# Kernel tuning notes

Hardware: AMD Instinct MI355X
Metric: run time of the kernel (lower is better)

The kernel has to match this reference:

```python
import jax, jax.numpy as jnp
import numpy as np

N_NODES = 50000
N_EDGES = 800000
HIDDEN = 100
NUM_TASKS = 128
NUM_GRAPHS = 2000
ATOM_DIMS = [119, 5, 12, 12, 10, 6, 6, 2, 2]  # OGB full_atom_feature_dims
EPS = 1e-16  # stands in for PyG's clamp(min=0) so that pow(-1) stays finite


def setup_inputs() -> dict:
    key = jax.random.key(0)
    ks = jax.random.split(key, 8)
    x = jax.random.randint(ks[0], (N_NODES, 9), 0, 2, dtype=jnp.int32)
    edge_index = jax.random.randint(ks[1], (2, N_EDGES), 0, N_NODES, dtype=jnp.int32)
    batch = jnp.sort(jax.random.randint(ks[2], (N_NODES,), 0, NUM_GRAPHS, dtype=jnp.int32))
    s = 1.0 / np.sqrt(HIDDEN)
    atom_emb = jax.random.normal(ks[3], (sum(ATOM_DIMS), HIDDEN), jnp.float32)
    W1 = jax.random.normal(ks[4], (HIDDEN, HIDDEN), jnp.float32) * s
    b1 = jnp.zeros((HIDDEN,), jnp.float32)
    W2 = jax.random.normal(ks[5], (HIDDEN, HIDDEN), jnp.float32) * s
    b2 = jnp.zeros((HIDDEN,), jnp.float32)
    Wlin = jax.random.normal(ks[6], (HIDDEN, NUM_TASKS), jnp.float32) * s
    blin = jnp.zeros((NUM_TASKS,), jnp.float32)
    return dict(x=x, edge_index=edge_index, batch=batch, atom_emb=atom_emb,
                W1=W1, b1=b1, W2=W2, b2=b2, Wlin=Wlin, blin=blin)


def reference(x, edge_index, batch, atom_emb, W1, b1, W2, b2, Wlin, blin):
    # --- AtomEncoder: sum of per-feature categorical embeddings ---
    offsets = jnp.asarray(np.concatenate([[0], np.cumsum(ATOM_DIMS)[:-1]]), jnp.int32)
    h = jnp.take(atom_emb, x + offsets[None, :], axis=0).sum(axis=1)  # [N, H]

    # --- GCN normalization with self-loops (gcn_norm, edge_weight=None) ---
    loops = jnp.arange(N_NODES, dtype=edge_index.dtype)
    row = jnp.concatenate([edge_index[0], loops])  # source
    col = jnp.concatenate([edge_index[1], loops])  # target
    ew = jnp.ones(row.shape[0], jnp.float32)
    deg = jax.ops.segment_sum(ew, col, num_segments=N_NODES)  # in-degree incl self-loop
    dinv = jnp.where(deg > 0, deg ** -0.5, 0.0)
    norm = dinv[row] * ew * dinv[col]  # [E+N]
    cnt = jnp.maximum(deg, 1.0)  # messages per target node (for mean)

    def gcn_conv(h, W, b):
        msg = norm[:, None] * (h @ W)[row]  # [E+N, H]
        # PowerMeanAggregation(p=-1): clamp(0,100).pow(-1) -> mean -> clamp(0,100).pow(-1)
        msg = jnp.clip(msg, EPS, 100.0) ** (-1.0)
        agg = jax.ops.segment_sum(msg, col, num_segments=N_NODES) / cnt[:, None]
        return jnp.clip(agg, EPS, 100.0) ** (-1.0) + b

    h = jax.nn.relu(gcn_conv(h, W1, b1))
    h = gcn_conv(h, W2, b2)

    # --- global_mean_pool over batch ---
    gcnt = jax.ops.segment_sum(jnp.ones((N_NODES,), jnp.float32), batch, num_segments=NUM_GRAPHS)
    pooled = jax.ops.segment_sum(h, batch, num_segments=NUM_GRAPHS) / jnp.maximum(gcnt, 1.0)[:, None]

    return pooled @ Wlin + blin  # [NUM_GRAPHS, NUM_TASKS]
```

## Files before the change

kernel.cpp:

```cpp
#include <hip/hip_runtime.h>

#define N_NODES   50000
#define N_EDGES   800000
#define HIDDEN    100
#define NUM_TASKS 128
#define NUM_GRAPHS 2000
#define EPS 1e-16f

static __device__ __forceinline__ float rcp_fast(float v) {
    return __builtin_amdgcn_rcpf(v);
}
static __device__ __forceinline__ float invclip(float v) {
    return rcp_fast(fminf(fmaxf(v, EPS), 100.0f));
}

__global__ void init_kernel(int* __restrict__ deg, int* __restrict__ cursor) {
    int i = blockIdx.x * blockDim.x + threadIdx.x;
    if (i < N_NODES) { deg[i] = 1; cursor[i] = 0; }
}

__global__ void deg_count_kernel(const int* __restrict__ col, int* __restrict__ deg) {
    int e = blockIdx.x * blockDim.x + threadIdx.x;
    if (e < N_EDGES) atomicAdd(&deg[col[e]], 1);
}

__global__ void blk_sum_kernel(const int* __restrict__ deg, int* __restrict__ bsum) {
    int i = blockIdx.x * 256 + threadIdx.x;
    int v = (i < N_NODES) ? (deg[i] - 1) : 0;
#pragma unroll
    for (int off = 32; off > 0; off >>= 1) v += __shfl_down(v, off, 64);
    __shared__ int ws[4];
    if ((threadIdx.x & 63) == 0) ws[threadIdx.x >> 6] = v;
    __syncthreads();
    if (threadIdx.x == 0) bsum[blockIdx.x] = ws[0] + ws[1] + ws[2] + ws[3];
}

__global__ void bsum_scan_kernel(int* __restrict__ bsum, int nblk) {
    __shared__ int buf[256];
    int t = threadIdx.x;
    int v = (t < nblk) ? bsum[t] : 0;
    buf[t] = v;
    __syncthreads();
    for (int off = 1; off < 256; off <<= 1) {
        int x = (t >= off) ? buf[t - off] : 0;
        __syncthreads();
        buf[t] += x;
        __syncthreads();
    }
    if (t < nblk) bsum[t] = buf[t] - v;
}

__global__ void blk_scan_kernel(const int* __restrict__ deg, const int* __restrict__ bbase,
                                int* __restrict__ csr_off, float* __restrict__ dinv) {
    __shared__ int buf[256];
    int t = threadIdx.x;
    int i = blockIdx.x * 256 + t;
    int dv = (i < N_NODES) ? deg[i] : 1;
    int v = (i < N_NODES) ? (dv - 1) : 0;
    buf[t] = v;
    __syncthreads();
    for (int off = 1; off < 256; off <<= 1) {
        int x = (t >= off) ? buf[t - off] : 0;
        __syncthreads();
        buf[t] += x;
        __syncthreads();
    }
    if (i < N_NODES) {
        csr_off[i] = bbase[blockIdx.x] + buf[t] - v;
        dinv[i] = 1.0f / sqrtf((float)dv);
    } else if (i == N_NODES) {
        csr_off[N_NODES] = N_EDGES;
    }
}

__global__ void scatter_kernel(const int* __restrict__ row, const int* __restrict__ col,
                               const int* __restrict__ csr_off, int* __restrict__ cursor,
                               const float* __restrict__ dinv, int2* __restrict__ csr_pack) {
    int e = blockIdx.x * blockDim.x + threadIdx.x;
    if (e >= N_EDGES) return;
    int s = row[e], d = col[e];
    int pos = csr_off[d] + atomicAdd(&cursor[d], 1);
    int2 p;
    p.x = s;
    p.y = __float_as_int(dinv[s] * dinv[d]);
    csr_pack[pos] = p;
}

__global__ void encoder_kernel(const int* __restrict__ x, const float* __restrict__ emb,
                               float* __restrict__ h) {
    int n = blockIdx.x;
    int d = threadIdx.x;
    if (d >= HIDDEN) return;
    const int offs[9] = {0, 119, 124, 136, 148, 158, 164, 170, 172};
    float acc = 0.0f;
#pragma unroll
    for (int f = 0; f < 9; ++f) {
        int idx = x[n * 9 + f] + offs[f];
        acc += emb[idx * HIDDEN + d];
    }
    h[n * HIDDEN + d] = acc;
}

#define MM_NODES 64
#define WL_PAD   10032
__global__ __launch_bounds__(512) void matmul_kernel(const float* __restrict__ h,
                                                     const float* __restrict__ W,
                                                     float* __restrict__ out) {
    __shared__ float Wl[WL_PAD];
    __shared__ float hl[MM_NODES * HIDDEN];
    int tid = threadIdx.x;
    int nb = blockIdx.x * MM_NODES;

    for (int i = tid; i < WL_PAD; i += 512)
        Wl[i] = (i < HIDDEN * HIDDEN) ? W[i] : 0.0f;
    for (int i = tid; i < MM_NODES * HIDDEN; i += 512) {
        int n = i / HIDDEN;
        hl[i] = (nb + n < N_NODES) ? h[(size_t)(nb + n) * HIDDEN + (i % HIDDEN)] : 0.0f;
    }
    __syncthreads();

    int tx = tid & 31;
    int ty = tid >> 5;

    float4 acc[4];
#pragma unroll
    for (int jn = 0; jn < 4; ++jn) acc[jn] = make_float4(0.f, 0.f, 0.f, 0.f);

    for (int kk = 0; kk < HIDDEN; kk += 4) {
        float hs[4][4];
#pragma unroll
        for (int jn = 0; jn < 4; ++jn) {
            float4 hv = *(const float4*)&hl[(ty + 16 * jn) * HIDDEN + kk];
            hs[jn][0] = hv.x; hs[jn][1] = hv.y; hs[jn][2] = hv.z; hs[jn][3] = hv.w;
        }
#pragma unroll
        for (int dk = 0; dk < 4; ++dk) {
            float4 wv = *(const float4*)&Wl[(kk + dk) * HIDDEN + 4 * tx];
#pragma unroll
            for (int jn = 0; jn < 4; ++jn) {
                acc[jn].x += hs[jn][dk] * wv.x;
                acc[jn].y += hs[jn][dk] * wv.y;
                acc[jn].z += hs[jn][dk] * wv.z;
                acc[jn].w += hs[jn][dk] * wv.w;
            }
        }
    }

    if (tx < 25) {
#pragma unroll
        for (int jn = 0; jn < 4; ++jn) {
            int n = nb + ty + 16 * jn;
            if (n < N_NODES)
                *(float4*)&out[(size_t)n * HIDDEN + 4 * tx] = acc[jn];
        }
    }
}

__global__ __launch_bounds__(256) void agg_kernel(
        const float* __restrict__ hw, const int* __restrict__ csr_off,
        const int2* __restrict__ csr_pack, const float* __restrict__ dinv,
        const int* __restrict__ deg, const float* __restrict__ bias,
        float* __restrict__ out, int relu) {
    int wid  = (blockIdx.x * blockDim.x + threadIdx.x) >> 6;
    int lane = threadIdx.x & 63;
    if (wid >= N_NODES) return;
    int n = wid;
    bool act = lane < 50;
    const float2* hw2 = (const float2*)hw;

    float cnt = (float)deg[n];
    float thr = 100.0f * cnt;

    float dn  = dinv[n];
    float nrm = dn * dn;
    float2 acc;
    if (act) {
        float2 v = hw2[(size_t)n * 50 + lane];
        acc.x = invclip(nrm * v.x);
        acc.y = invclip(nrm * v.y);
    } else {
        acc.x = 3.0e38f;
        acc.y = 3.0e38f;
    }

    int beg = csr_off[n], end = csr_off[n + 1];
    for (int i = beg; i < end; i += 8) {
        int2 p[8];
        float2 v[8];
#pragma unroll
        for (int j = 0; j < 8; ++j) {
            int idx = i + j;
            idx = (idx < end) ? idx : (end - 1);
            p[j] = csr_pack[idx];
        }
#pragma unroll
        for (int j = 0; j < 8; ++j)
            v[j] = act ? hw2[(size_t)p[j].x * 50 + lane] : make_float2(1.f, 1.f);
#pragma unroll
        for (int j = 0; j < 8; ++j) {
            if (i + j < end) {
                float w = __int_as_float(p[j].y);
                acc.x += invclip(w * v[j].x);
                acc.y += invclip(w * v[j].y);
            }
        }
        if (__all((acc.x >= thr) & (acc.y >= thr))) break;
    }

    if (act) {
        float rcnt = rcp_fast(cnt);
        float2 o;
        o.x = invclip(acc.x * rcnt) + bias[2 * lane];
        o.y = invclip(acc.y * rcnt) + bias[2 * lane + 1];
        if (relu) { o.x = fmaxf(o.x, 0.f); o.y = fmaxf(o.y, 0.f); }
        *(float2*)&out[(size_t)n * HIDDEN + 2 * lane] = o;
    }
}

__global__ void pool_final_kernel(const float* __restrict__ h, const int* __restrict__ batch,
                                  const float* __restrict__ Wlin, const float* __restrict__ blin,
                                  float* __restrict__ out) {
    int g = blockIdx.x;
    int t = threadIdx.x;
    __shared__ float pl[HIDDEN];

    int lo = 0, hi = N_NODES;
    while (lo < hi) { int mid = (lo + hi) >> 1; if (batch[mid] < g) lo = mid + 1; else hi = mid; }
    int start = lo;
    hi = N_NODES;
    while (lo < hi) { int mid = (lo + hi) >> 1; if (batch[mid] < g + 1) lo = mid + 1; else hi = mid; }
    int end = lo;

    float inv = 1.0f / fmaxf((float)(end - start), 1.0f);
    if (t < HIDDEN) {
        float acc = 0.f;
        for (int n = start; n < end; ++n) acc += h[(size_t)n * HIDDEN + t];
        pl[t] = acc * inv;
    }
    __syncthreads();

    float o = 0.f;
#pragma unroll 4
    for (int j = 0; j < HIDDEN; ++j) o += pl[j] * Wlin[j * NUM_TASKS + t];
    out[(size_t)g * NUM_TASKS + t] = o + blin[t];
}

extern "C" void kernel_launch(void* const* d_in, const int* in_sizes, int n_in,
                              void* d_out, int out_size, void* d_ws, size_t ws_size,
                              hipStream_t stream) {
    const int*   x     = (const int*)d_in[0];
    const int*   ei    = (const int*)d_in[1];
    const int*   batch = (const int*)d_in[2];
    const float* emb   = (const float*)d_in[3];
    const float* W1    = (const float*)d_in[4];
    const float* b1    = (const float*)d_in[5];
    const float* W2    = (const float*)d_in[6];
    const float* b2    = (const float*)d_in[7];
    const float* Wlin  = (const float*)d_in[8];
    const float* blin  = (const float*)d_in[9];
    float* out = (float*)d_out;

    const int* row = ei;
    const int* col = ei + N_EDGES;

    char* ws = (char*)d_ws;
    auto alloc = [&](size_t bytes) -> char* {
        char* p = ws;
        ws += (bytes + 255) & ~(size_t)255;
        return p;
    };
    int*   deg      = (int*)  alloc((size_t)N_NODES * 4);
    int*   cursor   = (int*)  alloc((size_t)N_NODES * 4);
    int*   csr_off  = (int*)  alloc((size_t)(N_NODES + 1) * 4);
    float* dinv     = (float*)alloc((size_t)N_NODES * 4);
    int2*  csr_pack = (int2*) alloc((size_t)N_EDGES * 8);
    float* bufA     = (float*)alloc((size_t)N_NODES * HIDDEN * 4);
    float* bufB     = (float*)alloc((size_t)N_NODES * HIDDEN * 4);
    int*   bsum     = (int*)  alloc(256 * 4);

    const int SCAN_BLOCKS = (N_NODES + 255) / 256;

    init_kernel<<<(N_NODES + 255) / 256, 256, 0, stream>>>(deg, cursor);
    deg_count_kernel<<<(N_EDGES + 255) / 256, 256, 0, stream>>>(col, deg);
    blk_sum_kernel<<<SCAN_BLOCKS, 256, 0, stream>>>(deg, bsum);
    bsum_scan_kernel<<<1, 256, 0, stream>>>(bsum, SCAN_BLOCKS);
    blk_scan_kernel<<<SCAN_BLOCKS, 256, 0, stream>>>(deg, bsum, csr_off, dinv);
    scatter_kernel<<<(N_EDGES + 255) / 256, 256, 0, stream>>>(row, col, csr_off, cursor, dinv,
                                                              csr_pack);
    encoder_kernel<<<N_NODES, 128, 0, stream>>>(x, emb, bufA);

    const int MM_BLOCKS = (N_NODES + MM_NODES - 1) / MM_NODES;
    matmul_kernel<<<MM_BLOCKS, 512, 0, stream>>>(bufA, W1, bufB);
    agg_kernel<<<(N_NODES + 3) / 4, 256, 0, stream>>>(bufB, csr_off, csr_pack,
                                                      dinv, deg, b1, bufA, 1);
    matmul_kernel<<<MM_BLOCKS, 512, 0, stream>>>(bufA, W2, bufB);
    agg_kernel<<<(N_NODES + 3) / 4, 256, 0, stream>>>(bufB, csr_off, csr_pack,
                                                      dinv, deg, b2, bufA, 0);

    pool_final_kernel<<<NUM_GRAPHS, 128, 0, stream>>>(bufA, batch, Wlin, blin, out);
}
```

Measured before the change: 324.7 us.

## Store features in 16-wide column-blocked layout and aggregate per feature block

Features are stored as 7 column blocks of 16 values, each laid out contiguously across all nodes. The aggregation now runs one wavefront per (block, node) pair, with four edge groups of 16 lanes each, and combines the partial sums by shuffle reduction. The aim is to make each gathered neighbour row 64 bytes, so a block's working set is small enough to stay cached, and to spread work across more wavefronts. The cost is that each CSR entry is read 7 times, blocks with fewer than 16 valid columns waste lanes, and the early-exit check now needs shuffles.

```diff
diff --git a/kernel.cpp b/kernel.cpp
--- a/kernel.cpp
+++ b/kernel.cpp
@@ -5,6 +5,7 @@
 #define HIDDEN    100
 #define NUM_TASKS 128
 #define NUM_GRAPHS 2000
+#define NBLK      7
 #define EPS 1e-16f
 
 static __device__ __forceinline__ float rcp_fast(float v) {
@@ -102,20 +103,27 @@
 }
 
 #define MM_NODES 64
+#define HL_W     112
 #define WL_PAD   10032
-__global__ __launch_bounds__(512) void matmul_kernel(const float* __restrict__ h,
+__global__ __launch_bounds__(512) void matmul_kernel(const float* __restrict__ in,
+                                                     int in_blocked,
                                                      const float* __restrict__ W,
-                                                     float* __restrict__ out) {
+                                                     float* __restrict__ outb) {
     __shared__ float Wl[WL_PAD];
-    __shared__ float hl[MM_NODES * HIDDEN];
+    __shared__ float hl[MM_NODES * HL_W];
     int tid = threadIdx.x;
     int nb = blockIdx.x * MM_NODES;
 
     for (int i = tid; i < WL_PAD; i += 512)
         Wl[i] = (i < HIDDEN * HIDDEN) ? W[i] : 0.0f;
-    for (int i = tid; i < MM_NODES * HIDDEN; i += 512) {
-        int n = i / HIDDEN;
-        hl[i] = (nb + n < N_NODES) ? h[(size_t)(nb + n) * HIDDEN + (i % HIDDEN)] : 0.0f;
+    for (int i = tid; i < MM_NODES * HL_W; i += 512) {
+        int n = i / HL_W, k = i % HL_W;
+        int gn = nb + n;
+        float v = 0.0f;
+        if (gn < N_NODES && k < HIDDEN)
+            v = in_blocked ? in[(((size_t)(k >> 4) * N_NODES + gn) << 4) + (k & 15)]
+                           : in[(size_t)gn * HIDDEN + k];
+        hl[i] = v;
     }
     __syncthreads();
 
@@ -130,7 +138,7 @@
         float hs[4][4];
 #pragma unroll
         for (int jn = 0; jn < 4; ++jn) {
-            float4 hv = *(const float4*)&hl[(ty + 16 * jn) * HIDDEN + kk];
+            float4 hv = *(const float4*)&hl[(ty + 16 * jn) * HL_W + kk];
             hs[jn][0] = hv.x; hs[jn][1] = hv.y; hs[jn][2] = hv.z; hs[jn][3] = hv.w;
         }
 #pragma unroll
@@ -147,77 +155,71 @@
     }
 
     if (tx < 25) {
+        int b = tx >> 2;
+        int d16 = (4 * tx) & 15;
 #pragma unroll
         for (int jn = 0; jn < 4; ++jn) {
             int n = nb + ty + 16 * jn;
             if (n < N_NODES)
-                *(float4*)&out[(size_t)n * HIDDEN + 4 * tx] = acc[jn];
+                *(float4*)&outb[(((size_t)b * N_NODES + n) << 4) + d16] = acc[jn];
         }
     }
 }
 
 __global__ __launch_bounds__(256) void agg_kernel(
-        const float* __restrict__ hw, const int* __restrict__ csr_off,
+        const float* __restrict__ hwb, const int* __restrict__ csr_off,
         const int2* __restrict__ csr_pack, const float* __restrict__ dinv,
         const int* __restrict__ deg, const float* __restrict__ bias,
-        float* __restrict__ out, int relu) {
-    int wid  = (blockIdx.x * blockDim.x + threadIdx.x) >> 6;
+        float* __restrict__ outb, int relu) {
+    int wid = (blockIdx.x * blockDim.x + threadIdx.x) >> 6;
+    if (wid >= NBLK * N_NODES) return;
+    int b = wid / N_NODES;
+    int n = wid - b * N_NODES;
     int lane = threadIdx.x & 63;
-    if (wid >= N_NODES) return;
-    int n = wid;
-    bool act = lane < 50;
-    const float2* hw2 = (const float2*)hw;
+    int eg = lane >> 4, d16 = lane & 15;
+    int d = (b << 4) + d16;
+    bool valid = d < HIDDEN;
 
     float cnt = (float)deg[n];
     float thr = 100.0f * cnt;
-
     float dn  = dinv[n];
     float nrm = dn * dn;
-    float2 acc;
-    if (act) {
-        float2 v = hw2[(size_t)n * 50 + lane];
-        acc.x = invclip(nrm * v.x);
-        acc.y = invclip(nrm * v.y);
+
+    const float* blk = hwb + (((size_t)b * N_NODES) << 4);
+
+    float acc;
+    if (eg == 0) {
+        if (valid) acc = invclip(nrm * blk[(n << 4) + d16]);
+        else       acc = 3.0e38f;
     } else {
-        acc.x = 3.0e38f;
-        acc.y = 3.0e38f;
+        acc = 0.0f;
     }
 
     int beg = csr_off[n], end = csr_off[n + 1];
-    for (int i = beg; i < end; i += 8) {
-        int2 p[8];
-        float2 v[8];
-#pragma unroll
-        for (int j = 0; j < 8; ++j) {
-            int idx = i + j;
-            idx = (idx < end) ? idx : (end - 1);
-            p[j] = csr_pack[idx];
+    for (int i = beg; i < end; i += 4) {
+        int idx = i + eg;
+        bool on = idx < end;
+        int2 p = csr_pack[on ? idx : (end - 1)];
+        float v = blk[(p.x << 4) + d16];
+        if (on & valid) acc += invclip(__int_as_float(p.y) * v);
+        if ((i - beg) & 4) {
+            float t = acc + __shfl_xor(acc, 16);
+            t += __shfl_xor(t, 32);
+            if (__all(t >= thr)) break;
         }
-#pragma unroll
-        for (int j = 0; j < 8; ++j)
-            v[j] = act ? hw2[(size_t)p[j].x * 50 + lane] : make_float2(1.f, 1.f);
-#pragma unroll
-        for (int j = 0; j < 8; ++j) {
-            if (i + j < end) {
-                float w = __int_as_float(p[j].y);
-                acc.x += invclip(w * v[j].x);
-                acc.y += invclip(w * v[j].y);
-            }
-        }
-        if (__all((acc.x >= thr) & (acc.y >= thr))) break;
-    }
-
-    if (act) {
-        float rcnt = rcp_fast(cnt);
-        float2 o;
-        o.x = invclip(acc.x * rcnt) + bias[2 * lane];
-        o.y = invclip(acc.y * rcnt) + bias[2 * lane + 1];
-        if (relu) { o.x = fmaxf(o.x, 0.f); o.y = fmaxf(o.y, 0.f); }
-        *(float2*)&out[(size_t)n * HIDDEN + 2 * lane] = o;
-    }
-}
-
-__global__ void pool_final_kernel(const float* __restrict__ h, const int* __restrict__ batch,
+    }
+
+    float tot = acc + __shfl_xor(acc, 16);
+    tot += __shfl_xor(tot, 32);
+
+    if (eg == 0 && valid) {
+        float o = invclip(tot * rcp_fast(cnt)) + bias[d];
+        if (relu) o = fmaxf(o, 0.f);
+        outb[(((size_t)b * N_NODES + n) << 4) + d16] = o;
+    }
+}
+
+__global__ void pool_final_kernel(const float* __restrict__ hb, const int* __restrict__ batch,
                                   const float* __restrict__ Wlin, const float* __restrict__ blin,
                                   float* __restrict__ out) {
     int g = blockIdx.x;
@@ -233,8 +235,9 @@
 
     float inv = 1.0f / fmaxf((float)(end - start), 1.0f);
     if (t < HIDDEN) {
+        const float* col = hb + (((size_t)(t >> 4) * N_NODES) << 4) + (t & 15);
         float acc = 0.f;
-        for (int n = start; n < end; ++n) acc += h[(size_t)n * HIDDEN + t];
+        for (int n = start; n < end; ++n) acc += col[(size_t)n << 4];
         pl[t] = acc * inv;
     }
     __syncthreads();
@@ -269,13 +272,14 @@
         ws += (bytes + 255) & ~(size_t)255;
         return p;
     };
+    const size_t BLK_ELEMS = (size_t)NBLK * N_NODES * 16;
     int*   deg      = (int*)  alloc((size_t)N_NODES * 4);
     int*   cursor   = (int*)  alloc((size_t)N_NODES * 4);
     int*   csr_off  = (int*)  alloc((size_t)(N_NODES + 1) * 4);
     float* dinv     = (float*)alloc((size_t)N_NODES * 4);
     int2*  csr_pack = (int2*) alloc((size_t)N_EDGES * 8);
-    float* bufA     = (float*)alloc((size_t)N_NODES * HIDDEN * 4);
-    float* bufB     = (float*)alloc((size_t)N_NODES * HIDDEN * 4);
+    float* bufR     = (float*)alloc(BLK_ELEMS * 4);
+    float* bufB     = (float*)alloc(BLK_ELEMS * 4);
     int*   bsum     = (int*)  alloc(256 * 4);
 
     const int SCAN_BLOCKS = (N_NODES + 255) / 256;
@@ -287,15 +291,17 @@
     blk_scan_kernel<<<SCAN_BLOCKS, 256, 0, stream>>>(deg, bsum, csr_off, dinv);
     scatter_kernel<<<(N_EDGES + 255) / 256, 256, 0, stream>>>(row, col, csr_off, cursor, dinv,
                                                               csr_pack);
-    encoder_kernel<<<N_NODES, 128, 0, stream>>>(x, emb, bufA);
-
-    const int MM_BLOCKS = (N_NODES + MM_NODES - 1) / MM_NODES;
-    matmul_kernel<<<MM_BLOCKS, 512, 0, stream>>>(bufA, W1, bufB);
-    agg_kernel<<<(N_NODES + 3) / 4, 256, 0, stream>>>(bufB, csr_off, csr_pack,
-                                                      dinv, deg, b1, bufA, 1);
-    matmul_kernel<<<MM_BLOCKS, 512, 0, stream>>>(bufA, W2, bufB);
-    agg_kernel<<<(N_NODES + 3) / 4, 256, 0, stream>>>(bufB, csr_off, csr_pack,
-                                                      dinv, deg, b2, bufA, 0);
-
-    pool_final_kernel<<<NUM_GRAPHS, 128, 0, stream>>>(bufA, batch, Wlin, blin, out);
-}
+    encoder_kernel<<<N_NODES, 128, 0, stream>>>(x, emb, bufR);
+
+    const int MM_BLOCKS  = (N_NODES + MM_NODES - 1) / MM_NODES;
+    const int AGG_BLOCKS = (NBLK * N_NODES + 3) / 4;
+
+    matmul_kernel<<<MM_BLOCKS, 512, 0, stream>>>(bufR, 0, W1, bufB);
+    agg_kernel<<<AGG_BLOCKS, 256, 0, stream>>>(bufB, csr_off, csr_pack,
+                                               dinv, deg, b1, bufR, 1);
+    matmul_kernel<<<MM_BLOCKS, 512, 0, stream>>>(bufR, 1, W2, bufB);
+    agg_kernel<<<AGG_BLOCKS, 256, 0, stream>>>(bufB, csr_off, csr_pack,
+                                               dinv, deg, b2, bufR, 0);
+
+    pool_final_kernel<<<NUM_GRAPHS, 128, 0, stream>>>(bufR, batch, Wlin, blin, out);
+}
```

New measurement: 541.2 us. 1.67x slower.
